# Kernel tuning notes

Measured on AMD Instinct MI355X. Metric: run time of the kernel, lower is better.

Reference implementation:

```python
import jax, jax.numpy as jnp
import numpy as np

N = 50000      # nodes
E = 400000     # edges
F = 64         # feature_size
H = 4          # heads
D = 16         # embedding_size (per-head dim)
HD = H * D     # concat hidden = 64
ED = 16        # edge_dim
L = 3          # model_layers (extra TransformerConv layers)
DN = 256       # dense_neurons
G = 128        # number of graphs in the batch
SCALE = float(1.0 / np.sqrt(D))


def setup_inputs() -> dict:
    key = jax.random.key(0)
    ks = jax.random.split(key, 40)

    def w(k, shape, fan_in):
        return jax.random.normal(k, shape, jnp.float32) / np.float32(np.sqrt(fan_in))

    inp = {}
    inp["x"] = jax.random.normal(ks[0], (N, F), jnp.float32)
    inp["edge_attr"] = jax.random.normal(ks[1], (E, ED), jnp.float32)
    inp["edge_index"] = jax.random.randint(ks[2], (2, E), 0, N)
    inp["batch"] = jnp.sort(jax.random.randint(ks[3], (N,), 0, G))

    # conv1: feature_size -> heads*embedding
    inp["Wq0"] = w(ks[4], (F, HD), F); inp["bq0"] = jnp.zeros((HD,), jnp.float32)
    inp["Wk0"] = w(ks[5], (F, HD), F); inp["bk0"] = jnp.zeros((HD,), jnp.float32)
    inp["Wv0"] = w(ks[6], (F, HD), F); inp["bv0"] = jnp.zeros((HD,), jnp.float32)
    inp["We0"] = w(ks[7], (ED, HD), ED)                      # lin_edge, no bias
    inp["Ws0"] = w(ks[8], (F, HD), F); inp["bs0"] = jnp.zeros((HD,), jnp.float32)  # lin_skip
    inp["Wb0"] = w(ks[9], (3 * HD, 1), 3 * HD)               # lin_beta, no bias

    # stacked layers 1..L: heads*embedding -> heads*embedding
    inp["Wq"] = w(ks[10], (L, HD, HD), HD); inp["bq"] = jnp.zeros((L, HD), jnp.float32)
    inp["Wk"] = w(ks[11], (L, HD, HD), HD); inp["bk"] = jnp.zeros((L, HD), jnp.float32)
    inp["Wv"] = w(ks[12], (L, HD, HD), HD); inp["bv"] = jnp.zeros((L, HD), jnp.float32)
    inp["We"] = w(ks[13], (L, ED, HD), ED)
    inp["Ws"] = w(ks[14], (L, HD, HD), HD); inp["bs"] = jnp.zeros((L, HD), jnp.float32)
    inp["Wb"] = w(ks[15], (L, 3 * HD, 1), 3 * HD)

    # MLP head: Linear(2*HD -> DN), Linear(DN -> 1)
    inp["Wlin"] = w(ks[16], (2 * HD, DN), 2 * HD); inp["blin"] = jnp.zeros((DN,), jnp.float32)
    inp["Wout"] = w(ks[17], (DN, 1), DN); inp["bout"] = jnp.zeros((1,), jnp.float32)
    return inp


def _tconv(x, edge_attr, src, dst, Wq, bq, Wk, bk, Wv, bv, We, Ws, bs, Wb):
    """PyG TransformerConv (concat=True, beta=True, edge_dim), eval mode (no dropout)."""
    n = x.shape[0]
    q = (x @ Wq + bq).reshape(n, H, D)
    k = (x @ Wk + bk).reshape(n, H, D)
    v = (x @ Wv + bv).reshape(n, H, D)
    e = (edge_attr @ We).reshape(-1, H, D)
    ke = k[src] + e                                   # [E,H,D] keys with edge feats
    ve = v[src] + e                                   # [E,H,D] values with edge feats
    logits = jnp.einsum('ehd,ehd->eh', q[dst], ke) * SCALE
    # segment softmax over incoming edges of each target node
    m = jax.ops.segment_max(logits, dst, num_segments=n)
    p = jnp.exp(logits - m[dst])
    s = jax.ops.segment_sum(p, dst, num_segments=n)
    a = p / (s[dst] + 1e-16)                          # [E,H]
    agg = jax.ops.segment_sum(a[:, :, None] * ve, dst, num_segments=n).reshape(n, HD)
    skip = x @ Ws + bs                                # root/skip transform
    beta = jax.nn.sigmoid(jnp.concatenate([agg, skip, agg - skip], axis=-1) @ Wb)
    return beta * skip + (1.0 - beta) * agg


def reference(x, edge_attr, edge_index, batch,
              Wq0, bq0, Wk0, bk0, Wv0, bv0, We0, Ws0, bs0, Wb0,
              Wq, bq, Wk, bk, Wv, bv, We, Ws, bs, Wb,
              Wlin, blin, Wout, bout):
    src, dst = edge_index[0], edge_index[1]
    h = jax.nn.relu(_tconv(x, edge_attr, src, dst,
                           Wq0, bq0, Wk0, bk0, Wv0, bv0, We0, Ws0, bs0, Wb0))
    for i in range(L):
        h = jax.nn.relu(_tconv(h, edge_attr, src, dst,
                               Wq[i], bq[i], Wk[i], bk[i], Wv[i], bv[i],
                               We[i], Ws[i], bs[i], Wb[i]))
    # global max pool (gmp) and global mean pool (gap)
    cnt = jax.ops.segment_sum(jnp.ones((h.shape[0],), h.dtype), batch, num_segments=G)
    gmax = jax.ops.segment_max(h, batch, num_segments=G)
    gmax = jnp.where(cnt[:, None] > 0, gmax, 0.0)
    gmean = jax.ops.segment_sum(h, batch, num_segments=G) / jnp.maximum(cnt[:, None], 1.0)
    z = jnp.concatenate([gmax, gmean], axis=-1) @ Wlin + blin
    return jax.nn.sigmoid(z @ Wout + bout)
```

## Files before the change

kernel.cpp:

```cpp
#include <hip/hip_runtime.h>
#include <math.h>

#define SCALEF 0.25f

typedef __attribute__((ext_vector_type(8))) short short8;
typedef __attribute__((ext_vector_type(4))) float f32x4;

__device__ __forceinline__ unsigned short f2bf(float x) {
  unsigned u = __float_as_uint(x);
  unsigned r = u + 0x7FFFu + ((u >> 16) & 1u);
  return (unsigned short)(r >> 16);
}
__device__ __forceinline__ float bf2f(unsigned short h) {
  return __uint_as_float(((unsigned)h) << 16);
}

__global__ void k_hist(const int* __restrict__ dst, int* __restrict__ counts, int E) {
  int i = blockIdx.x * 256 + threadIdx.x;
  if (i < E) atomicAdd(&counts[dst[i]], 1);
}

__global__ __launch_bounds__(1024) void k_scan1(const int* __restrict__ counts,
                                                int* __restrict__ excl,
                                                int* __restrict__ bsums, int n) {
  __shared__ int sd[1024];
  int t = threadIdx.x;
  int i = blockIdx.x * 1024 + t;
  int v = (i < n) ? counts[i] : 0;
  sd[t] = v;
  __syncthreads();
  for (int off = 1; off < 1024; off <<= 1) {
    int x = (t >= off) ? sd[t - off] : 0;
    __syncthreads();
    sd[t] += x;
    __syncthreads();
  }
  if (i < n) excl[i] = sd[t] - v;
  if (t == 1023) bsums[blockIdx.x] = sd[1023];
}

__global__ void k_scan2(int* bsums, int nb) {
  if (threadIdx.x == 0 && blockIdx.x == 0) {
    int run = 0;
    for (int i = 0; i < nb; ++i) { int v = bsums[i]; bsums[i] = run; run += v; }
  }
}

__global__ __launch_bounds__(1024) void k_scan3(int* __restrict__ rowptr, int* __restrict__ cursor,
                                                const int* __restrict__ bsums, int n, int Etot) {
  int i = blockIdx.x * 1024 + threadIdx.x;
  if (i < n) { int v = rowptr[i] + bsums[blockIdx.x]; rowptr[i] = v; cursor[i] = v; }
  if (i == 0) rowptr[n] = Etot;
}

__global__ void k_scatter(const int* __restrict__ dst, int* __restrict__ cursor,
                          int* __restrict__ colidx, int E) {
  int i = blockIdx.x * 256 + threadIdx.x;
  if (i < E) { int pos = atomicAdd(&cursor[dst[i]], 1); colidx[pos] = i; }
}

__global__ void k_perm(const int* __restrict__ colidx, const int* __restrict__ esrc,
                       const float* __restrict__ EA, int* __restrict__ esrcp,
                       float* __restrict__ EAp, int E) {
  int r = blockIdx.x * 256 + threadIdx.x;
  if (r >= E) return;
  const int eid = colidx[r];
  esrcp[r] = esrc[eid] * 128;
  const float4* s4 = (const float4*)(EA + ((size_t)eid << 4));
  float4* d4 = (float4*)(EAp + ((size_t)r << 4));
  d4[0] = s4[0]; d4[1] = s4[1]; d4[2] = s4[2]; d4[3] = s4[3];
}

__global__ __launch_bounds__(256) void k_wqt(
    const float* __restrict__ Wq0, const float* __restrict__ bq0, const float* __restrict__ We0,
    const float* __restrict__ Wq, const float* __restrict__ bq, const float* __restrict__ We,
    float* __restrict__ Wqt, float* __restrict__ bqt) {
  const int l = blockIdx.x;
  const float* wq = (l == 0) ? Wq0 : Wq + (l - 1) * 4096;
  const float* bv = (l == 0) ? bq0 : bq + (l - 1) * 64;
  const float* we = (l == 0) ? We0 : We + (l - 1) * 1024;
  float* out  = Wqt + l * 4096;
  float* outb = bqt + l * 64;
  const int t = threadIdx.x;
  const int r = t >> 2;
  const int hh = t & 3;
  float wqr[16];
  #pragma unroll
  for (int d = 0; d < 16; ++d) wqr[d] = wq[r * 64 + hh * 16 + d];
  #pragma unroll
  for (int bb = 0; bb < 16; ++bb) {
    float s = 0.f;
    #pragma unroll
    for (int d = 0; d < 16; ++d) s += wqr[d] * we[bb * 64 + hh * 16 + d];
    out[r * 64 + hh * 16 + bb] = s * SCALEF;
  }
  if (r == 0) {
    #pragma unroll
    for (int bb = 0; bb < 16; ++bb) {
      float s = 0.f;
      #pragma unroll
      for (int d = 0; d < 16; ++d) s += bv[hh * 16 + d] * we[bb * 64 + hh * 16 + d];
      outb[hh * 16 + bb] = s * SCALEF;
    }
  }
}

__global__ void k_wprep(
    const float* __restrict__ Wq0, const float* __restrict__ Wk0, const float* __restrict__ Wv0,
    const float* __restrict__ Ws0,
    const float* __restrict__ Wq, const float* __restrict__ Wk, const float* __restrict__ Wv,
    const float* __restrict__ Ws, const float* __restrict__ Wqt,
    const float* __restrict__ bq0, const float* __restrict__ bk0, const float* __restrict__ bv0,
    const float* __restrict__ bs0,
    const float* __restrict__ bq, const float* __restrict__ bk, const float* __restrict__ bv,
    const float* __restrict__ bs, const float* __restrict__ bqt,
    unsigned short* __restrict__ WT, float* __restrict__ bcat) {
  const int id = blockIdx.x * 256 + threadIdx.x;
  if (id >= 4 * 5 * 4096) return;
  const int l = id / 20480;
  const int rem = id - l * 20480;
  const int mat = rem >> 12;
  const int idx = rem & 4095;
  const int k = idx >> 6;
  const int c = idx & 63;
  float v;
  if (mat == 0)      v = (l == 0) ? Wq0[idx] : Wq[(l - 1) * 4096 + idx];
  else if (mat == 1) v = (l == 0) ? Wk0[idx] : Wk[(l - 1) * 4096 + idx];
  else if (mat == 2) v = (l == 0) ? Wv0[idx] : Wv[(l - 1) * 4096 + idx];
  else if (mat == 3) v = (l == 0) ? Ws0[idx] : Ws[(l - 1) * 4096 + idx];
  else               v = Wqt[l * 4096 + idx];
  WT[(size_t)(l * 5 + mat) * 4096 + c * 64 + k] = f2bf(v);
  if (k == 0) {
    float b;
    if (mat == 0)      b = (l == 0) ? bq0[c] : bq[(l - 1) * 64 + c];
    else if (mat == 1) b = (l == 0) ? bk0[c] : bk[(l - 1) * 64 + c];
    else if (mat == 2) b = (l == 0) ? bv0[c] : bv[(l - 1) * 64 + c];
    else if (mat == 3) b = (l == 0) ? bs0[c] : bs[(l - 1) * 64 + c];
    else               b = bqt[l * 64 + c];
    bcat[(l * 5 + mat) * 64 + c] = b;
  }
}

__global__ void k_xcast(const float* __restrict__ x, unsigned short* __restrict__ xb, int n4) {
  int i = blockIdx.x * 256 + threadIdx.x;
  if (i < n4) {
    float4 v = ((const float4*)x)[i];
    ushort4 o;
    o.x = f2bf(v.x); o.y = f2bf(v.y); o.z = f2bf(v.z); o.w = f2bf(v.w);
    ((ushort4*)xb)[i] = o;
  }
}

__global__ __launch_bounds__(256) void k_linm(
    const unsigned short* __restrict__ Xb, const unsigned short* __restrict__ WT,
    const float* __restrict__ bcat,
    unsigned short* __restrict__ Qb, unsigned short* __restrict__ Kb,
    unsigned short* __restrict__ Vb, float* __restrict__ S,
    unsigned short* __restrict__ Tb, int n) {
  const int lane = threadIdx.x & 63;
  const int gw = blockIdx.x * 4 + (threadIdx.x >> 6);
  const int ntr = n >> 4;
  if (gw >= ntr * 5) return;
  const int tile_r = gw / 5;
  const int mat = gw - tile_r * 5;
  const int r0 = tile_r << 4;

  const int c15 = lane & 15;
  const int kg = lane >> 4;

  const unsigned short* xrow = Xb + (size_t)(r0 + c15) * 64 + kg * 8;
  const short8 a0 = *(const short8*)(xrow);
  const short8 a1 = *(const short8*)(xrow + 32);

  const unsigned short* wb = WT + ((size_t)mat << 12) + (size_t)c15 * 64 + kg * 8;

  f32x4 acc0 = {0.f, 0.f, 0.f, 0.f}, acc1 = acc0, acc2 = acc0, acc3 = acc0;
  {
    short8 b0 = *(const short8*)(wb);
    short8 b1 = *(const short8*)(wb + 32);
    acc0 = __builtin_amdgcn_mfma_f32_16x16x32_bf16(a0, b0, acc0, 0, 0, 0);
    acc0 = __builtin_amdgcn_mfma_f32_16x16x32_bf16(a1, b1, acc0, 0, 0, 0);
  }
  {
    short8 b0 = *(const short8*)(wb + 16 * 64);
    short8 b1 = *(const short8*)(wb + 16 * 64 + 32);
    acc1 = __builtin_amdgcn_mfma_f32_16x16x32_bf16(a0, b0, acc1, 0, 0, 0);
    acc1 = __builtin_amdgcn_mfma_f32_16x16x32_bf16(a1, b1, acc1, 0, 0, 0);
  }
  {
    short8 b0 = *(const short8*)(wb + 32 * 64);
    short8 b1 = *(const short8*)(wb + 32 * 64 + 32);
    acc2 = __builtin_amdgcn_mfma_f32_16x16x32_bf16(a0, b0, acc2, 0, 0, 0);
    acc2 = __builtin_amdgcn_mfma_f32_16x16x32_bf16(a1, b1, acc2, 0, 0, 0);
  }
  {
    short8 b0 = *(const short8*)(wb + 48 * 64);
    short8 b1 = *(const short8*)(wb + 48 * 64 + 32);
    acc3 = __builtin_amdgcn_mfma_f32_16x16x32_bf16(a0, b0, acc3, 0, 0, 0);
    acc3 = __builtin_amdgcn_mfma_f32_16x16x32_bf16(a1, b1, acc3, 0, 0, 0);
  }

  const float* bb = bcat + mat * 64;
  const float bi0 = bb[c15], bi1 = bb[16 + c15], bi2 = bb[32 + c15], bi3 = bb[48 + c15];

  const int rbase = r0 + kg * 4;
  if (mat == 3) {
    float* O = S;
    #pragma unroll
    for (int reg = 0; reg < 4; ++reg) {
      const size_t ro = (size_t)(rbase + reg) * 64;
      O[ro + c15]      = acc0[reg] + bi0;
      O[ro + 16 + c15] = acc1[reg] + bi1;
      O[ro + 32 + c15] = acc2[reg] + bi2;
      O[ro + 48 + c15] = acc3[reg] + bi3;
    }
  } else {
    unsigned short* O = (mat == 0) ? Qb : (mat == 1) ? Kb : (mat == 2) ? Vb : Tb;
    #pragma unroll
    for (int reg = 0; reg < 4; ++reg) {
      const size_t ro = (size_t)(rbase + reg) * 64;
      O[ro + c15]      = f2bf(acc0[reg] + bi0);
      O[ro + 16 + c15] = f2bf(acc1[reg] + bi1);
      O[ro + 32 + c15] = f2bf(acc2[reg] + bi2);
      O[ro + 48 + c15] = f2bf(acc3[reg] + bi3);
    }
  }
}

#define LOADST(KK, VV, EE, jj) do {                                       \
    int jc_ = (jj) < mc ? (jj) : mc - 1;                                  \
    int off_ = __builtin_amdgcn_readlane(snv, jc_);                       \
    KK = *(const unsigned short*)(kbase + off_);                          \
    VV = *(const unsigned short*)(vbase + off_);                          \
    EE = eabase[(size_t)(c0 + jc_) << 4];                                 \
  } while (0)

#define COMPUTE(KK, VV, EE, jj) do {                                      \
    if ((jj) < mc) {                                                      \
      float pl = qv * bf2f(KK) + tl * EE;                                 \
      pl += __shfl_xor(pl, 1, 64);                                        \
      pl += __shfl_xor(pl, 2, 64);                                        \
      pl += __shfl_xor(pl, 4, 64);                                        \
      pl += __shfl_xor(pl, 8, 64);                                        \
      const float p = __expf(pl);                                         \
      ssum += p;                                                          \
      accv += p * bf2f(VV);                                               \
      accw += p * EE;                                                     \
    }                                                                     \
  } while (0)

__global__ __launch_bounds__(128, 6) void k_attn(
    const unsigned short* __restrict__ Qb, const unsigned short* __restrict__ Kb,
    const unsigned short* __restrict__ Vb, const unsigned short* __restrict__ Tb,
    const float* __restrict__ S, const float* __restrict__ EAp,
    const int* __restrict__ esrcp, const int* __restrict__ rowptr,
    const float* __restrict__ We, const float* __restrict__ Wb,
    unsigned short* __restrict__ Hout, int n) {
  const int t = threadIdx.x;
  const int lane = t & 63;
  const int node = blockIdx.x * 2 + (t >> 6);
  if (node >= n) return;

  const float qv = bf2f(Qb[(size_t)node * 64 + lane]) * SCALEF;
  const float tl = bf2f(Tb[(size_t)node * 64 + lane]);
  const int r0 = rowptr[node], r1 = rowptr[node + 1];

  const char* kbase = (const char*)Kb + 2 * lane;
  const char* vbase = (const char*)Vb + 2 * lane;
  const float* eabase = EAp + (lane & 15);

  float ssum = 0.f, accv = 0.f, accw = 0.f;

  for (int c0 = r0; c0 < r1; c0 += 64) {
    const int mc = min(64, r1 - c0);
    int snv = 0;
    if (lane < mc) snv = esrcp[c0 + lane];

    unsigned short kA, vA, kB, vB, kC, vC, kD, vD;
    float eA, eB, eC, eD;
    LOADST(kA, vA, eA, 0);
    LOADST(kB, vB, eB, 1);
    LOADST(kC, vC, eC, 2);
    LOADST(kD, vD, eD, 3);

    for (int j = 0; j < mc; j += 4) {
      COMPUTE(kA, vA, eA, j);     LOADST(kA, vA, eA, j + 4);
      COMPUTE(kB, vB, eB, j + 1); LOADST(kB, vB, eB, j + 5);
      COMPUTE(kC, vC, eC, j + 2); LOADST(kC, vC, eC, j + 6);
      COMPUTE(kD, vD, eD, j + 3); LOADST(kD, vD, eD, j + 7);
    }
  }

  float agg = accv;
  #pragma unroll
  for (int j = 0; j < 16; ++j) {
    const float wj = __shfl(accw, (lane & 48) | j, 64);
    agg += wj * We[j * 64 + lane];
  }
  agg /= (ssum + 1e-16f);

  const float sk = S[(size_t)node * 64 + lane];
  float contrib = agg * Wb[lane] + sk * Wb[64 + lane] + (agg - sk) * Wb[128 + lane];
  #pragma unroll
  for (int off = 1; off < 64; off <<= 1) contrib += __shfl_xor(contrib, off, 64);
  const float beta = 1.f / (1.f + __expf(-contrib));
  const float o = beta * sk + (1.f - beta) * agg;
  Hout[(size_t)node * 64 + lane] = f2bf(fmaxf(o, 0.f));
}

__global__ __launch_bounds__(256) void k_pool(const unsigned short* __restrict__ Hf,
    const int* __restrict__ batch,
    float* __restrict__ gmax, float* __restrict__ gmean, int n) {
  const int g = blockIdx.x;
  const int lane = threadIdx.x & 63;
  const int w = threadIdx.x >> 6;

  int a = 0, b = n;
  while (a < b) { int mid = (a + b) >> 1; if (batch[mid] < g) a = mid + 1; else b = mid; }
  const int lo = a;
  b = n;
  while (a < b) { int mid = (a + b) >> 1; if (batch[mid] < g + 1) a = mid + 1; else b = mid; }
  const int hi = a;

  float vmax = -1e30f, vsum = 0.f;
  for (int i = lo + w; i < hi; i += 4) {
    const float v = bf2f(Hf[(size_t)i * 64 + lane]);
    vmax = fmaxf(vmax, v);
    vsum += v;
  }
  __shared__ float smax[4][64], ssum[4][64];
  smax[w][lane] = vmax;
  ssum[w][lane] = vsum;
  __syncthreads();
  if (w == 0) {
    const float mx = fmaxf(fmaxf(smax[0][lane], smax[1][lane]),
                           fmaxf(smax[2][lane], smax[3][lane]));
    const float sm = ssum[0][lane] + ssum[1][lane] + ssum[2][lane] + ssum[3][lane];
    const int cnt = hi - lo;
    gmax[g * 64 + lane]  = (cnt > 0) ? mx : 0.f;
    gmean[g * 64 + lane] = sm / fmaxf((float)cnt, 1.f);
  }
}

__global__ __launch_bounds__(256) void k_mlp(const float* __restrict__ gmax,
    const float* __restrict__ gmean,
    const float* __restrict__ Wlin, const float* __restrict__ blin,
    const float* __restrict__ Wout, const float* __restrict__ bout,
    float* __restrict__ out, int G) {
  __shared__ float cat[128];
  __shared__ float red[4];
  const int g = blockIdx.x;
  const int t = threadIdx.x;
  if (t < 64) cat[t] = gmax[g * 64 + t];
  else if (t < 128) cat[t] = gmean[g * 64 + (t - 64)];
  __syncthreads();
  float acc = blin[t];
  for (int j = 0; j < 128; ++j) acc += cat[j] * Wlin[j * 256 + t];
  float p = acc * Wout[t];
  #pragma unroll
  for (int off = 1; off < 64; off <<= 1) p += __shfl_xor(p, off, 64);
  if ((t & 63) == 0) red[t >> 6] = p;
  __syncthreads();
  if (t == 0) {
    const float z = red[0] + red[1] + red[2] + red[3] + bout[0];
    out[g] = 1.f / (1.f + __expf(-z));
  }
}

extern "C" void kernel_launch(void* const* d_in, const int* in_sizes, int n_in,
                              void* d_out, int out_size, void* d_ws, size_t ws_size,
                              hipStream_t stream) {
  const float* x     = (const float*)d_in[0];
  const float* ea    = (const float*)d_in[1];
  const int*   eidx  = (const int*)d_in[2];
  const int*   batch = (const int*)d_in[3];
  const float *Wq0 = (const float*)d_in[4],  *bq0 = (const float*)d_in[5];
  const float *Wk0 = (const float*)d_in[6],  *bk0 = (const float*)d_in[7];
  const float *Wv0 = (const float*)d_in[8],  *bv0 = (const float*)d_in[9];
  const float *We0 = (const float*)d_in[10];
  const float *Ws0 = (const float*)d_in[11], *bs0 = (const float*)d_in[12];
  const float *Wb0 = (const float*)d_in[13];
  const float *Wq  = (const float*)d_in[14], *bq  = (const float*)d_in[15];
  const float *Wk  = (const float*)d_in[16], *bk  = (const float*)d_in[17];
  const float *Wv  = (const float*)d_in[18], *bv  = (const float*)d_in[19];
  const float *We  = (const float*)d_in[20];
  const float *Ws  = (const float*)d_in[21], *bs  = (const float*)d_in[22];
  const float *Wb  = (const float*)d_in[23];
  const float *Wlin = (const float*)d_in[24], *blin = (const float*)d_in[25];
  const float *Wout = (const float*)d_in[26], *bout = (const float*)d_in[27];

  const int N = in_sizes[0] / 64;
  const int E = in_sizes[2] / 2;
  const int G = out_size;
  const int* esrc = eidx;
  const int* edst = eidx + E;

  char* wsp = (char*)d_ws;
  auto alloc = [&](size_t bytes) -> void* {
    void* p = (void*)wsp;
    wsp += (bytes + 255) & ~(size_t)255;
    return p;
  };
  unsigned short* Qb = (unsigned short*)alloc((size_t)N * 64 * 2);
  unsigned short* Kb = (unsigned short*)alloc((size_t)N * 64 * 2);
  unsigned short* Vb = (unsigned short*)alloc((size_t)N * 64 * 2);
  unsigned short* Tb = (unsigned short*)alloc((size_t)N * 64 * 2);
  float* Sb = (float*)alloc((size_t)N * 64 * 4);
  unsigned short* Hb16 = (unsigned short*)alloc((size_t)N * 64 * 2);
  unsigned short* Xb16 = (unsigned short*)alloc((size_t)N * 64 * 2);
  int* counts  = (int*)alloc((size_t)N * 4);
  int* rowptr  = (int*)alloc((size_t)(N + 1) * 4);
  int* cursor  = (int*)alloc((size_t)N * 4);
  int* colidx  = (int*)alloc((size_t)E * 4);
  int* bsums   = (int*)alloc(1024 * 4);
  int* esrcp   = (int*)alloc((size_t)E * 4);
  float* EAp   = (float*)alloc((size_t)E * 64);
  float* Wqt   = (float*)alloc(4 * 4096 * 4);
  float* bqt   = (float*)alloc(4 * 64 * 4);
  unsigned short* WT = (unsigned short*)alloc(4 * 5 * 4096 * 2);
  float* bcat  = (float*)alloc(4 * 5 * 64 * 4);
  float* gmaxf  = (float*)alloc((size_t)G * 64 * 4);
  float* gmeanf = (float*)alloc((size_t)G * 64 * 4);

  const int gridE = (E + 255) / 256;
  const int NB1 = (N + 1023) / 1024;
  hipMemsetAsync(counts, 0, (size_t)N * 4, stream);
  k_hist<<<gridE, 256, 0, stream>>>(edst, counts, E);
  k_scan1<<<NB1, 1024, 0, stream>>>(counts, rowptr, bsums, N);
  k_scan2<<<1, 64, 0, stream>>>(bsums, NB1);
  k_scan3<<<NB1, 1024, 0, stream>>>(rowptr, cursor, bsums, N, E);
  k_scatter<<<gridE, 256, 0, stream>>>(edst, cursor, colidx, E);
  k_perm<<<gridE, 256, 0, stream>>>(colidx, esrc, ea, esrcp, EAp, E);
  k_wqt<<<4, 256, 0, stream>>>(Wq0, bq0, We0, Wq, bq, We, Wqt, bqt);
  k_wprep<<<(4 * 5 * 4096 + 255) / 256, 256, 0, stream>>>(
      Wq0, Wk0, Wv0, Ws0, Wq, Wk, Wv, Ws, Wqt,
      bq0, bk0, bv0, bs0, bq, bk, bv, bs, bqt, WT, bcat);
  k_xcast<<<(N * 16 + 255) / 256, 256, 0, stream>>>(x, Xb16, N * 16);

  const int gridLinM = (((N >> 4) * 5) + 3) / 4;
  const int gridAttn = (N + 1) / 2;
  for (int l = 0; l < 4; ++l) {
    const float* we_ = (l == 0) ? We0 : We + (l - 1) * 1024;
    const float* wb_ = (l == 0) ? Wb0 : Wb + (l - 1) * 192;
    const unsigned short* xin = (l == 0) ? Xb16 : Hb16;
    k_linm<<<gridLinM, 256, 0, stream>>>(xin, WT + (size_t)l * 20480, bcat + l * 320,
                                         Qb, Kb, Vb, Sb, Tb, N);
    k_attn<<<gridAttn, 128, 0, stream>>>(Qb, Kb, Vb, Tb, Sb, EAp, esrcp, rowptr,
                                         we_, wb_, Hb16, N);
  }

  k_pool<<<G, 256, 0, stream>>>(Hb16, batch, gmaxf, gmeanf, N);
  k_mlp<<<G, 256, 0, stream>>>(gmaxf, gmeanf, Wlin, blin, Wout, bout,
                               (float*)d_out, G);
}
```

Measured before the change: 403.6 us.

## Compute all five projections per tile in linm; persistent-grid attention with hoisted weights

k_linm now has each wave load its 16-row input tile once and compute all five projection matrices in a loop, where before each (tile, matrix) pair had its own wave. This removes the redundant input loads but cuts wave-level parallelism by five. k_attn becomes a grid-stride persistent kernel: 256-thread blocks, grid capped at 1536, and the We/Wb weights held in registers once per wave. Its edge prefetch pipeline is also deepened from 4 to 6 in-flight gathers, which raises register pressure.

```diff
diff --git a/kernel.cpp b/kernel.cpp
--- a/kernel.cpp
+++ b/kernel.cpp
@@ -158,71 +158,69 @@
     unsigned short* __restrict__ Vb, float* __restrict__ S,
     unsigned short* __restrict__ Tb, int n) {
   const int lane = threadIdx.x & 63;
-  const int gw = blockIdx.x * 4 + (threadIdx.x >> 6);
+  const int tile = blockIdx.x * 4 + (threadIdx.x >> 6);
   const int ntr = n >> 4;
-  if (gw >= ntr * 5) return;
-  const int tile_r = gw / 5;
-  const int mat = gw - tile_r * 5;
-  const int r0 = tile_r << 4;
-
+  if (tile >= ntr) return;
+  const int r0 = tile << 4;
   const int c15 = lane & 15;
   const int kg = lane >> 4;
+  const int rbase = r0 + kg * 4;
 
   const unsigned short* xrow = Xb + (size_t)(r0 + c15) * 64 + kg * 8;
   const short8 a0 = *(const short8*)(xrow);
   const short8 a1 = *(const short8*)(xrow + 32);
 
-  const unsigned short* wb = WT + ((size_t)mat << 12) + (size_t)c15 * 64 + kg * 8;
-
-  f32x4 acc0 = {0.f, 0.f, 0.f, 0.f}, acc1 = acc0, acc2 = acc0, acc3 = acc0;
-  {
-    short8 b0 = *(const short8*)(wb);
-    short8 b1 = *(const short8*)(wb + 32);
-    acc0 = __builtin_amdgcn_mfma_f32_16x16x32_bf16(a0, b0, acc0, 0, 0, 0);
-    acc0 = __builtin_amdgcn_mfma_f32_16x16x32_bf16(a1, b1, acc0, 0, 0, 0);
-  }
-  {
-    short8 b0 = *(const short8*)(wb + 16 * 64);
-    short8 b1 = *(const short8*)(wb + 16 * 64 + 32);
-    acc1 = __builtin_amdgcn_mfma_f32_16x16x32_bf16(a0, b0, acc1, 0, 0, 0);
-    acc1 = __builtin_amdgcn_mfma_f32_16x16x32_bf16(a1, b1, acc1, 0, 0, 0);
-  }
-  {
-    short8 b0 = *(const short8*)(wb + 32 * 64);
-    short8 b1 = *(const short8*)(wb + 32 * 64 + 32);
-    acc2 = __builtin_amdgcn_mfma_f32_16x16x32_bf16(a0, b0, acc2, 0, 0, 0);
-    acc2 = __builtin_amdgcn_mfma_f32_16x16x32_bf16(a1, b1, acc2, 0, 0, 0);
-  }
-  {
-    short8 b0 = *(const short8*)(wb + 48 * 64);
-    short8 b1 = *(const short8*)(wb + 48 * 64 + 32);
-    acc3 = __builtin_amdgcn_mfma_f32_16x16x32_bf16(a0, b0, acc3, 0, 0, 0);
-    acc3 = __builtin_amdgcn_mfma_f32_16x16x32_bf16(a1, b1, acc3, 0, 0, 0);
-  }
-
-  const float* bb = bcat + mat * 64;
-  const float bi0 = bb[c15], bi1 = bb[16 + c15], bi2 = bb[32 + c15], bi3 = bb[48 + c15];
-
-  const int rbase = r0 + kg * 4;
-  if (mat == 3) {
-    float* O = S;
-    #pragma unroll
-    for (int reg = 0; reg < 4; ++reg) {
-      const size_t ro = (size_t)(rbase + reg) * 64;
-      O[ro + c15]      = acc0[reg] + bi0;
-      O[ro + 16 + c15] = acc1[reg] + bi1;
-      O[ro + 32 + c15] = acc2[reg] + bi2;
-      O[ro + 48 + c15] = acc3[reg] + bi3;
-    }
-  } else {
-    unsigned short* O = (mat == 0) ? Qb : (mat == 1) ? Kb : (mat == 2) ? Vb : Tb;
-    #pragma unroll
-    for (int reg = 0; reg < 4; ++reg) {
-      const size_t ro = (size_t)(rbase + reg) * 64;
-      O[ro + c15]      = f2bf(acc0[reg] + bi0);
-      O[ro + 16 + c15] = f2bf(acc1[reg] + bi1);
-      O[ro + 32 + c15] = f2bf(acc2[reg] + bi2);
-      O[ro + 48 + c15] = f2bf(acc3[reg] + bi3);
+  #pragma unroll
+  for (int mat = 0; mat < 5; ++mat) {
+    const unsigned short* wb = WT + ((size_t)mat << 12) + (size_t)c15 * 64 + kg * 8;
+    f32x4 acc0 = {0.f, 0.f, 0.f, 0.f}, acc1 = acc0, acc2 = acc0, acc3 = acc0;
+    {
+      short8 b0 = *(const short8*)(wb);
+      short8 b1 = *(const short8*)(wb + 32);
+      acc0 = __builtin_amdgcn_mfma_f32_16x16x32_bf16(a0, b0, acc0, 0, 0, 0);
+      acc0 = __builtin_amdgcn_mfma_f32_16x16x32_bf16(a1, b1, acc0, 0, 0, 0);
+    }
+    {
+      short8 b0 = *(const short8*)(wb + 16 * 64);
+      short8 b1 = *(const short8*)(wb + 16 * 64 + 32);
+      acc1 = __builtin_amdgcn_mfma_f32_16x16x32_bf16(a0, b0, acc1, 0, 0, 0);
+      acc1 = __builtin_amdgcn_mfma_f32_16x16x32_bf16(a1, b1, acc1, 0, 0, 0);
+    }
+    {
+      short8 b0 = *(const short8*)(wb + 32 * 64);
+      short8 b1 = *(const short8*)(wb + 32 * 64 + 32);
+      acc2 = __builtin_amdgcn_mfma_f32_16x16x32_bf16(a0, b0, acc2, 0, 0, 0);
+      acc2 = __builtin_amdgcn_mfma_f32_16x16x32_bf16(a1, b1, acc2, 0, 0, 0);
+    }
+    {
+      short8 b0 = *(const short8*)(wb + 48 * 64);
+      short8 b1 = *(const short8*)(wb + 48 * 64 + 32);
+      acc3 = __builtin_amdgcn_mfma_f32_16x16x32_bf16(a0, b0, acc3, 0, 0, 0);
+      acc3 = __builtin_amdgcn_mfma_f32_16x16x32_bf16(a1, b1, acc3, 0, 0, 0);
+    }
+
+    const float* bb = bcat + mat * 64;
+    const float bi0 = bb[c15], bi1 = bb[16 + c15], bi2 = bb[32 + c15], bi3 = bb[48 + c15];
+
+    if (mat == 3) {
+      #pragma unroll
+      for (int reg = 0; reg < 4; ++reg) {
+        const size_t ro = (size_t)(rbase + reg) * 64;
+        S[ro + c15]      = acc0[reg] + bi0;
+        S[ro + 16 + c15] = acc1[reg] + bi1;
+        S[ro + 32 + c15] = acc2[reg] + bi2;
+        S[ro + 48 + c15] = acc3[reg] + bi3;
+      }
+    } else {
+      unsigned short* O = (mat == 0) ? Qb : (mat == 1) ? Kb : (mat == 2) ? Vb : Tb;
+      #pragma unroll
+      for (int reg = 0; reg < 4; ++reg) {
+        const size_t ro = (size_t)(rbase + reg) * 64;
+        O[ro + c15]      = f2bf(acc0[reg] + bi0);
+        O[ro + 16 + c15] = f2bf(acc1[reg] + bi1);
+        O[ro + 32 + c15] = f2bf(acc2[reg] + bi2);
+        O[ro + 48 + c15] = f2bf(acc3[reg] + bi3);
+      }
     }
   }
 }
@@ -249,7 +247,7 @@
     }                                                                     \
   } while (0)
 
-__global__ __launch_bounds__(128, 6) void k_attn(
+__global__ __launch_bounds__(256, 6) void k_attn(
     const unsigned short* __restrict__ Qb, const unsigned short* __restrict__ Kb,
     const unsigned short* __restrict__ Vb, const unsigned short* __restrict__ Tb,
     const float* __restrict__ S, const float* __restrict__ EAp,
@@ -258,54 +256,65 @@
     unsigned short* __restrict__ Hout, int n) {
   const int t = threadIdx.x;
   const int lane = t & 63;
-  const int node = blockIdx.x * 2 + (t >> 6);
-  if (node >= n) return;
-
-  const float qv = bf2f(Qb[(size_t)node * 64 + lane]) * SCALEF;
-  const float tl = bf2f(Tb[(size_t)node * 64 + lane]);
-  const int r0 = rowptr[node], r1 = rowptr[node + 1];
+  const int wid = t >> 6;
+
+  float wer[16];
+  #pragma unroll
+  for (int j = 0; j < 16; ++j) wer[j] = We[j * 64 + lane];
+  const float wb0 = Wb[lane], wb1 = Wb[64 + lane], wb2 = Wb[128 + lane];
 
   const char* kbase = (const char*)Kb + 2 * lane;
   const char* vbase = (const char*)Vb + 2 * lane;
   const float* eabase = EAp + (lane & 15);
 
-  float ssum = 0.f, accv = 0.f, accw = 0.f;
-
-  for (int c0 = r0; c0 < r1; c0 += 64) {
-    const int mc = min(64, r1 - c0);
-    int snv = 0;
-    if (lane < mc) snv = esrcp[c0 + lane];
-
-    unsigned short kA, vA, kB, vB, kC, vC, kD, vD;
-    float eA, eB, eC, eD;
-    LOADST(kA, vA, eA, 0);
-    LOADST(kB, vB, eB, 1);
-    LOADST(kC, vC, eC, 2);
-    LOADST(kD, vD, eD, 3);
-
-    for (int j = 0; j < mc; j += 4) {
-      COMPUTE(kA, vA, eA, j);     LOADST(kA, vA, eA, j + 4);
-      COMPUTE(kB, vB, eB, j + 1); LOADST(kB, vB, eB, j + 5);
-      COMPUTE(kC, vC, eC, j + 2); LOADST(kC, vC, eC, j + 6);
-      COMPUTE(kD, vD, eD, j + 3); LOADST(kD, vD, eD, j + 7);
-    }
-  }
-
-  float agg = accv;
-  #pragma unroll
-  for (int j = 0; j < 16; ++j) {
-    const float wj = __shfl(accw, (lane & 48) | j, 64);
-    agg += wj * We[j * 64 + lane];
-  }
-  agg /= (ssum + 1e-16f);
-
-  const float sk = S[(size_t)node * 64 + lane];
-  float contrib = agg * Wb[lane] + sk * Wb[64 + lane] + (agg - sk) * Wb[128 + lane];
-  #pragma unroll
-  for (int off = 1; off < 64; off <<= 1) contrib += __shfl_xor(contrib, off, 64);
-  const float beta = 1.f / (1.f + __expf(-contrib));
-  const float o = beta * sk + (1.f - beta) * agg;
-  Hout[(size_t)node * 64 + lane] = f2bf(fmaxf(o, 0.f));
+  const int stride = gridDim.x * 4;
+  for (int node = blockIdx.x * 4 + wid; node < n; node += stride) {
+    const float qv = bf2f(Qb[(size_t)node * 64 + lane]) * SCALEF;
+    const float tl = bf2f(Tb[(size_t)node * 64 + lane]);
+    const int r0 = rowptr[node], r1 = rowptr[node + 1];
+
+    float ssum = 0.f, accv = 0.f, accw = 0.f;
+
+    for (int c0 = r0; c0 < r1; c0 += 64) {
+      const int mc = min(64, r1 - c0);
+      int snv = 0;
+      if (lane < mc) snv = esrcp[c0 + lane];
+
+      unsigned short kA, vA, kB, vB, kC, vC, kD, vD, kE, vE, kF, vF;
+      float eA, eB, eC, eD, eE, eF;
+      LOADST(kA, vA, eA, 0);
+      LOADST(kB, vB, eB, 1);
+      LOADST(kC, vC, eC, 2);
+      LOADST(kD, vD, eD, 3);
+      LOADST(kE, vE, eE, 4);
+      LOADST(kF, vF, eF, 5);
+
+      for (int j = 0; j < mc; j += 6) {
+        COMPUTE(kA, vA, eA, j);     LOADST(kA, vA, eA, j + 6);
+        COMPUTE(kB, vB, eB, j + 1); LOADST(kB, vB, eB, j + 7);
+        COMPUTE(kC, vC, eC, j + 2); LOADST(kC, vC, eC, j + 8);
+        COMPUTE(kD, vD, eD, j + 3); LOADST(kD, vD, eD, j + 9);
+        COMPUTE(kE, vE, eE, j + 4); LOADST(kE, vE, eE, j + 10);
+        COMPUTE(kF, vF, eF, j + 5); LOADST(kF, vF, eF, j + 11);
+      }
+    }
+
+    float agg = accv;
+    #pragma unroll
+    for (int j = 0; j < 16; ++j) {
+      const float wj = __shfl(accw, (lane & 48) | j, 64);
+      agg += wj * wer[j];
+    }
+    agg /= (ssum + 1e-16f);
+
+    const float sk = S[(size_t)node * 64 + lane];
+    float contrib = agg * wb0 + sk * wb1 + (agg - sk) * wb2;
+    #pragma unroll
+    for (int off = 1; off < 64; off <<= 1) contrib += __shfl_xor(contrib, off, 64);
+    const float beta = 1.f / (1.f + __expf(-contrib));
+    const float o = beta * sk + (1.f - beta) * agg;
+    Hout[(size_t)node * 64 + lane] = f2bf(fmaxf(o, 0.f));
+  }
 }
 
 __global__ __launch_bounds__(256) void k_pool(const unsigned short* __restrict__ Hf,
@@ -437,15 +446,16 @@
       bq0, bk0, bv0, bs0, bq, bk, bv, bs, bqt, WT, bcat);
   k_xcast<<<(N * 16 + 255) / 256, 256, 0, stream>>>(x, Xb16, N * 16);
 
-  const int gridLinM = (((N >> 4) * 5) + 3) / 4;
-  const int gridAttn = (N + 1) / 2;
+  const int gridLinM = ((N >> 4) + 3) / 4;
+  int gridAttn = (N + 3) / 4;
+  if (gridAttn > 1536) gridAttn = 1536;
   for (int l = 0; l < 4; ++l) {
     const float* we_ = (l == 0) ? We0 : We + (l - 1) * 1024;
     const float* wb_ = (l == 0) ? Wb0 : Wb + (l - 1) * 192;
     const unsigned short* xin = (l == 0) ? Xb16 : Hb16;
     k_linm<<<gridLinM, 256, 0, stream>>>(xin, WT + (size_t)l * 20480, bcat + l * 320,
                                          Qb, Kb, Vb, Sb, Tb, N);
-    k_attn<<<gridAttn, 128, 0, stream>>>(Qb, Kb, Vb, Tb, Sb, EAp, esrcp, rowptr,
+    k_attn<<<gridAttn, 256, 0, stream>>>(Qb, Kb, Vb, Tb, Sb, EAp, esrcp, rowptr,
                                          we_, wb_, Hb16, N);
   }
 
```

After: 443.4 us. 1.1x slower.

## Store edge attributes and skip projection in bf16, compute all five mats per warp

Applied to the files above, without the earlier changes.

The permuted edge attributes are stored as bf16 instead of fp32, which halves the per-edge gather traffic in the attention kernel. The skip projection S is also written as bf16. The linear kernel now has each warp compute all five weight matrices for one 16-row tile, so the X fragment is loaded once instead of five times. The cost is lower precision in the edge term and the skip path, plus fewer, longer-running warps in the linear kernel.

```diff
diff --git a/kernel.cpp b/kernel.cpp
--- a/kernel.cpp
+++ b/kernel.cpp
@@ -61,14 +61,20 @@
 
 __global__ void k_perm(const int* __restrict__ colidx, const int* __restrict__ esrc,
                        const float* __restrict__ EA, int* __restrict__ esrcp,
-                       float* __restrict__ EAp, int E) {
+                       unsigned short* __restrict__ EAp, int E) {
   int r = blockIdx.x * 256 + threadIdx.x;
   if (r >= E) return;
   const int eid = colidx[r];
   esrcp[r] = esrc[eid] * 128;
   const float4* s4 = (const float4*)(EA + ((size_t)eid << 4));
-  float4* d4 = (float4*)(EAp + ((size_t)r << 4));
-  d4[0] = s4[0]; d4[1] = s4[1]; d4[2] = s4[2]; d4[3] = s4[3];
+  float4 a = s4[0], b = s4[1], c = s4[2], d = s4[3];
+  union { unsigned short us[16]; uint4 u4[2]; } o;
+  o.us[0] = f2bf(a.x); o.us[1] = f2bf(a.y); o.us[2] = f2bf(a.z); o.us[3] = f2bf(a.w);
+  o.us[4] = f2bf(b.x); o.us[5] = f2bf(b.y); o.us[6] = f2bf(b.z); o.us[7] = f2bf(b.w);
+  o.us[8] = f2bf(c.x); o.us[9] = f2bf(c.y); o.us[10] = f2bf(c.z); o.us[11] = f2bf(c.w);
+  o.us[12] = f2bf(d.x); o.us[13] = f2bf(d.y); o.us[14] = f2bf(d.z); o.us[15] = f2bf(d.w);
+  uint4* d4 = (uint4*)(EAp + ((size_t)r << 4));
+  d4[0] = o.u4[0]; d4[1] = o.u4[1];
 }
 
 __global__ __launch_bounds__(256) void k_wqt(
@@ -155,67 +161,55 @@
     const unsigned short* __restrict__ Xb, const unsigned short* __restrict__ WT,
     const float* __restrict__ bcat,
     unsigned short* __restrict__ Qb, unsigned short* __restrict__ Kb,
-    unsigned short* __restrict__ Vb, float* __restrict__ S,
+    unsigned short* __restrict__ Vb, unsigned short* __restrict__ Sb,
     unsigned short* __restrict__ Tb, int n) {
   const int lane = threadIdx.x & 63;
-  const int gw = blockIdx.x * 4 + (threadIdx.x >> 6);
+  const int tile = blockIdx.x * 4 + (threadIdx.x >> 6);
   const int ntr = n >> 4;
-  if (gw >= ntr * 5) return;
-  const int tile_r = gw / 5;
-  const int mat = gw - tile_r * 5;
-  const int r0 = tile_r << 4;
-
+  if (tile >= ntr) return;
+  const int r0 = tile << 4;
   const int c15 = lane & 15;
   const int kg = lane >> 4;
+  const int rbase = r0 + kg * 4;
 
   const unsigned short* xrow = Xb + (size_t)(r0 + c15) * 64 + kg * 8;
   const short8 a0 = *(const short8*)(xrow);
   const short8 a1 = *(const short8*)(xrow + 32);
 
-  const unsigned short* wb = WT + ((size_t)mat << 12) + (size_t)c15 * 64 + kg * 8;
-
-  f32x4 acc0 = {0.f, 0.f, 0.f, 0.f}, acc1 = acc0, acc2 = acc0, acc3 = acc0;
-  {
-    short8 b0 = *(const short8*)(wb);
-    short8 b1 = *(const short8*)(wb + 32);
-    acc0 = __builtin_amdgcn_mfma_f32_16x16x32_bf16(a0, b0, acc0, 0, 0, 0);
-    acc0 = __builtin_amdgcn_mfma_f32_16x16x32_bf16(a1, b1, acc0, 0, 0, 0);
-  }
-  {
-    short8 b0 = *(const short8*)(wb + 16 * 64);
-    short8 b1 = *(const short8*)(wb + 16 * 64 + 32);
-    acc1 = __builtin_amdgcn_mfma_f32_16x16x32_bf16(a0, b0, acc1, 0, 0, 0);
-    acc1 = __builtin_amdgcn_mfma_f32_16x16x32_bf16(a1, b1, acc1, 0, 0, 0);
-  }
-  {
-    short8 b0 = *(const short8*)(wb + 32 * 64);
-    short8 b1 = *(const short8*)(wb + 32 * 64 + 32);
-    acc2 = __builtin_amdgcn_mfma_f32_16x16x32_bf16(a0, b0, acc2, 0, 0, 0);
-    acc2 = __builtin_amdgcn_mfma_f32_16x16x32_bf16(a1, b1, acc2, 0, 0, 0);
-  }
-  {
-    short8 b0 = *(const short8*)(wb + 48 * 64);
-    short8 b1 = *(const short8*)(wb + 48 * 64 + 32);
-    acc3 = __builtin_amdgcn_mfma_f32_16x16x32_bf16(a0, b0, acc3, 0, 0, 0);
-    acc3 = __builtin_amdgcn_mfma_f32_16x16x32_bf16(a1, b1, acc3, 0, 0, 0);
-  }
-
-  const float* bb = bcat + mat * 64;
-  const float bi0 = bb[c15], bi1 = bb[16 + c15], bi2 = bb[32 + c15], bi3 = bb[48 + c15];
-
-  const int rbase = r0 + kg * 4;
-  if (mat == 3) {
-    float* O = S;
-    #pragma unroll
-    for (int reg = 0; reg < 4; ++reg) {
-      const size_t ro = (size_t)(rbase + reg) * 64;
-      O[ro + c15]      = acc0[reg] + bi0;
-      O[ro + 16 + c15] = acc1[reg] + bi1;
-      O[ro + 32 + c15] = acc2[reg] + bi2;
-      O[ro + 48 + c15] = acc3[reg] + bi3;
-    }
-  } else {
-    unsigned short* O = (mat == 0) ? Qb : (mat == 1) ? Kb : (mat == 2) ? Vb : Tb;
+  #pragma unroll
+  for (int mat = 0; mat < 5; ++mat) {
+    const unsigned short* wb = WT + ((size_t)mat << 12) + (size_t)c15 * 64 + kg * 8;
+    f32x4 acc0 = {0.f, 0.f, 0.f, 0.f}, acc1 = acc0, acc2 = acc0, acc3 = acc0;
+    {
+      short8 b0 = *(const short8*)(wb);
+      short8 b1 = *(const short8*)(wb + 32);
+      acc0 = __builtin_amdgcn_mfma_f32_16x16x32_bf16(a0, b0, acc0, 0, 0, 0);
+      acc0 = __builtin_amdgcn_mfma_f32_16x16x32_bf16(a1, b1, acc0, 0, 0, 0);
+    }
+    {
+      short8 b0 = *(const short8*)(wb + 16 * 64);
+      short8 b1 = *(const short8*)(wb + 16 * 64 + 32);
+      acc1 = __builtin_amdgcn_mfma_f32_16x16x32_bf16(a0, b0, acc1, 0, 0, 0);
+      acc1 = __builtin_amdgcn_mfma_f32_16x16x32_bf16(a1, b1, acc1, 0, 0, 0);
+    }
+    {
+      short8 b0 = *(const short8*)(wb + 32 * 64);
+      short8 b1 = *(const short8*)(wb + 32 * 64 + 32);
+      acc2 = __builtin_amdgcn_mfma_f32_16x16x32_bf16(a0, b0, acc2, 0, 0, 0);
+      acc2 = __builtin_amdgcn_mfma_f32_16x16x32_bf16(a1, b1, acc2, 0, 0, 0);
+    }
+    {
+      short8 b0 = *(const short8*)(wb + 48 * 64);
+      short8 b1 = *(const short8*)(wb + 48 * 64 + 32);
+      acc3 = __builtin_amdgcn_mfma_f32_16x16x32_bf16(a0, b0, acc3, 0, 0, 0);
+      acc3 = __builtin_amdgcn_mfma_f32_16x16x32_bf16(a1, b1, acc3, 0, 0, 0);
+    }
+
+    const float* bb = bcat + mat * 64;
+    const float bi0 = bb[c15], bi1 = bb[16 + c15], bi2 = bb[32 + c15], bi3 = bb[48 + c15];
+
+    unsigned short* O = (mat == 0) ? Qb : (mat == 1) ? Kb : (mat == 2) ? Vb
+                      : (mat == 3) ? Sb : Tb;
     #pragma unroll
     for (int reg = 0; reg < 4; ++reg) {
       const size_t ro = (size_t)(rbase + reg) * 64;
@@ -237,7 +231,8 @@
 
 #define COMPUTE(KK, VV, EE, jj) do {                                      \
     if ((jj) < mc) {                                                      \
-      float pl = qv * bf2f(KK) + tl * EE;                                 \
+      const float ef = bf2f(EE);                                          \
+      float pl = qv * bf2f(KK) + tl * ef;                                 \
       pl += __shfl_xor(pl, 1, 64);                                        \
       pl += __shfl_xor(pl, 2, 64);                                        \
       pl += __shfl_xor(pl, 4, 64);                                        \
@@ -245,14 +240,14 @@
       const float p = __expf(pl);                                         \
       ssum += p;                                                          \
       accv += p * bf2f(VV);                                               \
-      accw += p * EE;                                                     \
+      accw += p * ef;                                                     \
     }                                                                     \
   } while (0)
 
 __global__ __launch_bounds__(128, 6) void k_attn(
     const unsigned short* __restrict__ Qb, const unsigned short* __restrict__ Kb,
     const unsigned short* __restrict__ Vb, const unsigned short* __restrict__ Tb,
-    const float* __restrict__ S, const float* __restrict__ EAp,
+    const unsigned short* __restrict__ Sb, const unsigned short* __restrict__ EAp,
     const int* __restrict__ esrcp, const int* __restrict__ rowptr,
     const float* __restrict__ We, const float* __restrict__ Wb,
     unsigned short* __restrict__ Hout, int n) {
@@ -267,7 +262,7 @@
 
   const char* kbase = (const char*)Kb + 2 * lane;
   const char* vbase = (const char*)Vb + 2 * lane;
-  const float* eabase = EAp + (lane & 15);
+  const unsigned short* eabase = EAp + (lane & 15);
 
   float ssum = 0.f, accv = 0.f, accw = 0.f;
 
@@ -277,7 +272,7 @@
     if (lane < mc) snv = esrcp[c0 + lane];
 
     unsigned short kA, vA, kB, vB, kC, vC, kD, vD;
-    float eA, eB, eC, eD;
+    unsigned short eA, eB, eC, eD;
     LOADST(kA, vA, eA, 0);
     LOADST(kB, vB, eB, 1);
     LOADST(kC, vC, eC, 2);
@@ -299,7 +294,7 @@
   }
   agg /= (ssum + 1e-16f);
 
-  const float sk = S[(size_t)node * 64 + lane];
+  const float sk = bf2f(Sb[(size_t)node * 64 + lane]);
   float contrib = agg * Wb[lane] + sk * Wb[64 + lane] + (agg - sk) * Wb[128 + lane];
   #pragma unroll
   for (int off = 1; off < 64; off <<= 1) contrib += __shfl_xor(contrib, off, 64);
@@ -405,7 +400,7 @@
   unsigned short* Kb = (unsigned short*)alloc((size_t)N * 64 * 2);
   unsigned short* Vb = (unsigned short*)alloc((size_t)N * 64 * 2);
   unsigned short* Tb = (unsigned short*)alloc((size_t)N * 64 * 2);
-  float* Sb = (float*)alloc((size_t)N * 64 * 4);
+  unsigned short* Sb16 = (unsigned short*)alloc((size_t)N * 64 * 2);
   unsigned short* Hb16 = (unsigned short*)alloc((size_t)N * 64 * 2);
   unsigned short* Xb16 = (unsigned short*)alloc((size_t)N * 64 * 2);
   int* counts  = (int*)alloc((size_t)N * 4);
@@ -414,7 +409,7 @@
   int* colidx  = (int*)alloc((size_t)E * 4);
   int* bsums   = (int*)alloc(1024 * 4);
   int* esrcp   = (int*)alloc((size_t)E * 4);
-  float* EAp   = (float*)alloc((size_t)E * 64);
+  unsigned short* EAp = (unsigned short*)alloc((size_t)E * 16 * 2);
   float* Wqt   = (float*)alloc(4 * 4096 * 4);
   float* bqt   = (float*)alloc(4 * 64 * 4);
   unsigned short* WT = (unsigned short*)alloc(4 * 5 * 4096 * 2);
@@ -437,15 +432,15 @@
       bq0, bk0, bv0, bs0, bq, bk, bv, bs, bqt, WT, bcat);
   k_xcast<<<(N * 16 + 255) / 256, 256, 0, stream>>>(x, Xb16, N * 16);
 
-  const int gridLinM = (((N >> 4) * 5) + 3) / 4;
+  const int gridLinM = ((N >> 4) + 3) / 4;
   const int gridAttn = (N + 1) / 2;
   for (int l = 0; l < 4; ++l) {
     const float* we_ = (l == 0) ? We0 : We + (l - 1) * 1024;
     const float* wb_ = (l == 0) ? Wb0 : Wb + (l - 1) * 192;
     const unsigned short* xin = (l == 0) ? Xb16 : Hb16;
     k_linm<<<gridLinM, 256, 0, stream>>>(xin, WT + (size_t)l * 20480, bcat + l * 320,
-                                         Qb, Kb, Vb, Sb, Tb, N);
-    k_attn<<<gridAttn, 128, 0, stream>>>(Qb, Kb, Vb, Tb, Sb, EAp, esrcp, rowptr,
+                                         Qb, Kb, Vb, Sb16, Tb, N);
+    k_attn<<<gridAttn, 128, 0, stream>>>(Qb, Kb, Vb, Tb, Sb16, EAp, esrcp, rowptr,
                                          we_, wb_, Hb16, N);
   }
 
```

Measured after the change: 408.2 us. No clear change (+1.1%).
